# Kernel tuning notes

Hardware: AMD Instinct MI355X
Metric: run time of the kernel (lower is better)

Reference implementation:

```python
import jax, jax.numpy as jnp
import numpy as np

S, U, K, N_NEG, Z_DIM, C_DIM, LENGTH = 8, 8, 6, 17, 64, 256, 512
T = LENGTH + K


def setup_inputs() -> dict:
    key = jax.random.key(0)
    k1, k2, k3, k4, k5, k6 = jax.random.split(key, 6)
    z = jax.random.normal(k1, (S * U, T, Z_DIM), dtype=jnp.float32)
    c = jax.random.normal(k2, (S * U, T, C_DIM), dtype=jnp.float32)
    W = jax.random.normal(k3, (K, Z_DIM, C_DIM), dtype=jnp.float32) * 0.02
    b = jax.random.normal(k4, (K, Z_DIM), dtype=jnp.float32) * 0.02
    # torch: randint(0, U) per step
    batch_index = jax.random.randint(k5, (K, U, N_NEG), 0, U, dtype=jnp.int32)
    # torch: randint(1, length) + arange(length), mod length  (negative != positive at same pos)
    base = jax.random.randint(k6, (K, S, U, N_NEG, LENGTH), 1, LENGTH, dtype=jnp.int32)
    seq_index = (base + jnp.arange(LENGTH, dtype=jnp.int32)) % LENGTH
    return {"z": z, "c": c, "W": W, "b": b,
            "batch_index": batch_index, "seq_index": seq_index}


def reference(z, c, W, b, batch_index, seq_index):
    K_, zdim, _ = W.shape
    U_, n_neg = batch_index.shape[1], batch_index.shape[2]
    S_ = seq_index.shape[1]
    length = z.shape[1] - K_
    scale = 1.0 / float(np.sqrt(zdim))

    z_r = z.reshape(S_, U_, -1, zdim)              # [S,U,T,Z]
    c_s = c[:, :-K_, :].reshape(S_, U_, length, -1)  # [S,U,L,C]
    sp = jnp.arange(S_)[:, None, None, None]        # speaker index broadcast

    losses, accs = [], []
    for k in range(K_):  # fixed small number of prediction steps
        zs = z_r[:, :, k + 1:length + k + 1, :]                     # [S,U,L,Z]
        Wc = jnp.einsum('sulc,zc->sulz', c_s, W[k]) + b[k]          # predictor k
        f_pos = jnp.einsum('sulz,sulz->sul', zs, Wc) * scale        # [S,U,L]
        bi = batch_index[k][None, :, :, None]                       # [1,U,N,1]
        si = seq_index[k]                                           # [S,U,N,L]
        z_neg = zs[sp, bi, si, :]                                   # [S,U,N,L,Z]
        f_neg = jnp.einsum('sunlz,sulz->sunl', z_neg, Wc) * scale   # [S,U,N,L]
        f = jnp.concatenate([f_pos[:, :, None, :], f_neg], axis=2)  # [S,U,N+1,L]
        # cross entropy with label 0 along class axis
        losses.append(jnp.mean(jax.nn.logsumexpp(f, axis=2) if False else jax.nn.logsumexp(f, axis=2) - f_pos))
        accs.append(jnp.mean((jnp.argmax(f, axis=2) == 0).astype(jnp.float32)))

    loss = jnp.stack(losses).mean()
    return loss, jnp.stack(accs)
```

## Files before the change

### kernel.cpp

```cpp
#include <hip/hip_runtime.h>
#include <math.h>

#define S_N 8
#define U_N 8
#define K_N 6
#define NNEG 17
#define ZDIM 64
#define CDIM 256
#define LEN 512
#define TDIM (LEN + K_N)

typedef __attribute__((ext_vector_type(8))) short short8;
typedef __attribute__((ext_vector_type(4))) short short4v;
typedef __attribute__((ext_vector_type(4))) float f32x4;

__device__ __forceinline__ short f2bf(float x) {
    unsigned u = __builtin_bit_cast(unsigned, x);
    return (short)((u + 0x7fffu + ((u >> 16) & 1u)) >> 16);
}
__device__ __forceinline__ float bf2f(short h) {
    unsigned u = ((unsigned)(unsigned short)h) << 16;
    return __builtin_bit_cast(float, u);
}
__device__ __forceinline__ short8 cvt8(f32x4 a, f32x4 b) {
    short8 r;
    r[0] = f2bf(a[0]); r[1] = f2bf(a[1]); r[2] = f2bf(a[2]); r[3] = f2bf(a[3]);
    r[4] = f2bf(b[0]); r[5] = f2bf(b[1]); r[6] = f2bf(b[2]); r[7] = f2bf(b[3]);
    return r;
}


__global__ __launch_bounds__(256, 3) void cpc_gemm(
    const float* __restrict__ cg_, const float* __restrict__ Wg,
    const float* __restrict__ bg, short* __restrict__ Wcg)
{
    __shared__ __align__(16) short wlds[ZDIM * CDIM];
    __shared__ float wc[64][68];

    const int tid = threadIdx.x;
    const int bid = blockIdx.x;
    const int su  = bid >> 3;
    const int lt8 = bid & 7;
    const int l0  = lt8 * 64;

    const int wave   = tid >> 6;
    const int lane   = tid & 63;
    const int lane15 = lane & 15;
    const int lgrp   = lane >> 4;

    short8 af0, af1, af2, af3, af4, af5, af6, af7;
    {
        const int lrow = l0 + wave * 16 + lane15;
        const float* arow = cg_ + ((size_t)(su * TDIM + lrow)) * CDIM;
#define LDA(KC, AF) { \
        f32x4 a0_ = __builtin_nontemporal_load((const f32x4*)(arow + (KC) * 32 + lgrp * 8)); \
        f32x4 a1_ = __builtin_nontemporal_load((const f32x4*)(arow + (KC) * 32 + lgrp * 8 + 4)); \
        AF = cvt8(a0_, a1_); }
        LDA(0, af0) LDA(1, af1) LDA(2, af2) LDA(3, af3)
        LDA(4, af4) LDA(5, af5) LDA(6, af6) LDA(7, af7)
#undef LDA
    }

    for (int k = 0; k < K_N; ++k) {
        {
            const float* wbase = Wg + (size_t)k * ZDIM * CDIM;
            #pragma unroll
            for (int it = 0; it < 16; ++it) {
                int off = it * 1024 + tid * 4;
                int r = off >> 8;
                int c = off & 255;
                f32x4 v = *(const f32x4*)(wbase + off);
                short4v h;
                h.x = f2bf(v[0]); h.y = f2bf(v[1]); h.z = f2bf(v[2]); h.w = f2bf(v[3]);
                int chb = c >> 3;
                int hh  = (c >> 2) & 1;
                *(short4v*)&wlds[r * 256 + ((chb ^ (r & 7)) << 3) + hh * 4] = h;
            }
        }
        __syncthreads();

        {
            f32x4 acc0 = {0.f,0.f,0.f,0.f}, acc1 = {0.f,0.f,0.f,0.f};
            f32x4 acc2 = {0.f,0.f,0.f,0.f}, acc3 = {0.f,0.f,0.f,0.f};
            const int swb = lane15 & 7;
            const short* wl = &wlds[lane15 * 256];
#define DOKC(KC, AF) { \
            const int so = ((((KC) * 4 + lgrp) ^ swb) << 3); \
            acc0 = __builtin_amdgcn_mfma_f32_16x16x32_bf16(AF, *(const short8*)(wl + so),          acc0, 0, 0, 0); \
            acc1 = __builtin_amdgcn_mfma_f32_16x16x32_bf16(AF, *(const short8*)(wl + 16*256 + so), acc1, 0, 0, 0); \
            acc2 = __builtin_amdgcn_mfma_f32_16x16x32_bf16(AF, *(const short8*)(wl + 32*256 + so), acc2, 0, 0, 0); \
            acc3 = __builtin_amdgcn_mfma_f32_16x16x32_bf16(AF, *(const short8*)(wl + 48*256 + so), acc3, 0, 0, 0); }
            DOKC(0, af0) DOKC(1, af1) DOKC(2, af2) DOKC(3, af3)
            DOKC(4, af4) DOKC(5, af5) DOKC(6, af6) DOKC(7, af7)
#undef DOKC
            const int wrow = wave * 16 + lgrp * 4;
#define WCW(N, ACC) { \
            float bias_ = bg[k * ZDIM + (N) * 16 + lane15]; \
            wc[wrow + 0][(N) * 16 + lane15] = ACC[0] + bias_; \
            wc[wrow + 1][(N) * 16 + lane15] = ACC[1] + bias_; \
            wc[wrow + 2][(N) * 16 + lane15] = ACC[2] + bias_; \
            wc[wrow + 3][(N) * 16 + lane15] = ACC[3] + bias_; }
            WCW(0, acc0) WCW(1, acc1) WCW(2, acc2) WCW(3, acc3)
#undef WCW
        }
        __syncthreads();

        {
            const int row = tid >> 2;
            const int q   = tid & 3;
            f32x4 v0 = *(const f32x4*)&wc[row][q * 16];
            f32x4 v1 = *(const f32x4*)&wc[row][q * 16 + 4];
            f32x4 v2 = *(const f32x4*)&wc[row][q * 16 + 8];
            f32x4 v3 = *(const f32x4*)&wc[row][q * 16 + 12];
            short8 s0 = cvt8(v0, v1);
            short8 s1 = cvt8(v2, v3);
            short* dst = Wcg + (((size_t)(k * 64 + su) * LEN) + (l0 + row)) * ZDIM + q * 16;
            *(short8*)dst = s0;
            *(short8*)(dst + 8) = s1;
        }
    }
}


__global__ __launch_bounds__(256) void cpc_loss(
    const float* __restrict__ zg, const short* __restrict__ Wcg,
    const int* __restrict__ bidx, const int* __restrict__ sidx,
    float* __restrict__ bins)
{
    __shared__ int bi_sh[NNEG];
    __shared__ int si_sh[16 * NNEG];
    __shared__ float red[8];

    const int tid = threadIdx.x;
    const int bid = blockIdx.x;
    const int s   = bid & 7;
    const int b2  = bid >> 3;
    const int lt  = b2 & 31;
    const int u   = (b2 >> 5) & 7;
    const int k   = b2 >> 8;
    const int l0  = lt * 16;
    const int su  = s * 8 + u;

    if (tid < NNEG) bi_sh[tid] = bidx[(k * U_N + u) * NNEG + tid];
    for (int i = tid; i < 16 * NNEG; i += 256) {
        int lr = i / NNEG;
        int n  = i - lr * NNEG;
        si_sh[i] = sidx[((((size_t)k * S_N + s) * U_N + u) * NNEG + n) * LEN + (l0 + lr)];
    }
    __syncthreads();

    const int lrow = tid >> 4;
    const int c4   = tid & 15;
    const int l    = l0 + lrow;

    f32x4 wcv;
    {
        const short* wrow = Wcg + (((size_t)(k * 64 + su) * LEN) + l) * ZDIM + c4 * 4;
        short4v wb = __builtin_nontemporal_load((const short4v*)wrow);
        wcv[0] = bf2f(wb.x); wcv[1] = bf2f(wb.y); wcv[2] = bf2f(wb.z); wcv[3] = bf2f(wb.w);
    }

    float f0 = 0.f, mneg = -1e30f, se = 0.f;
    #pragma unroll 6
    for (int j = 0; j < 18; ++j) {
        size_t zrow;
        if (j == 0) {
            zrow = (size_t)su * TDIM + (k + 1 + l);
        } else {
            int n  = j - 1;
            int bi = bi_sh[n];
            int si = si_sh[lrow * NNEG + n];
            zrow = (size_t)(s * 8 + bi) * TDIM + (k + 1 + si);
        }
        f32x4 zv = *(const f32x4*)(zg + zrow * ZDIM + c4 * 4);
        float p = zv[0] * wcv[0];
        p = fmaf(zv[1], wcv[1], p);
        p = fmaf(zv[2], wcv[2], p);
        p = fmaf(zv[3], wcv[3], p);
        p += __shfl_xor(p, 1);
        p += __shfl_xor(p, 2);
        p += __shfl_xor(p, 4);
        p += __shfl_xor(p, 8);
        float f = p * 0.125f;
        if (j == 0) f0 = f; else mneg = fmaxf(mneg, f);
        se += __expf(f - 4.0f);
    }

    float lossv = (4.0f + __logf(se)) - f0;
    float accv  = (f0 >= mneg) ? 1.f : 0.f;
    if (c4 != 0) { lossv = 0.f; accv = 0.f; }
    lossv += __shfl_xor(lossv, 16); lossv += __shfl_xor(lossv, 32);
    accv  += __shfl_xor(accv, 16);  accv  += __shfl_xor(accv, 32);

    const int wave = tid >> 6;
    const int lane = tid & 63;
    if (lane == 0) { red[wave * 2] = lossv; red[wave * 2 + 1] = accv; }
    __syncthreads();
    if (tid == 0) atomicAdd(&bins[bid & 127], red[0] + red[2] + red[4] + red[6]);
    if (tid == 1) atomicAdd(&bins[128 + k * 128 + (bid & 127)],
                            red[1] + red[3] + red[5] + red[7]);
}

__global__ void cpc_final(const float* __restrict__ bins, float* __restrict__ out)
{
    const int lane = threadIdx.x;
    float v = bins[lane] + bins[lane + 64];
    #pragma unroll
    for (int off = 1; off < 64; off <<= 1) v += __shfl_xor(v, off);
    if (lane == 0) out[0] = v * (1.0f / 196608.0f);
    #pragma unroll
    for (int k = 0; k < K_N; ++k) {
        const float* bk = bins + 128 + k * 128;
        float a = bk[lane] + bk[lane + 64];
        #pragma unroll
        for (int off = 1; off < 64; off <<= 1) a += __shfl_xor(a, off);
        if (lane == 0) out[1 + k] = a * (1.0f / 32768.0f);
    }
}

__global__ __launch_bounds__(256, 3) void cpc_fused(
    const float* __restrict__ zg, const float* __restrict__ cg_,
    const float* __restrict__ Wg, const float* __restrict__ bg,
    const int* __restrict__ bidx, const int* __restrict__ sidx,
    float* __restrict__ out)
{
    __shared__ __align__(16) short wlds[ZDIM * CDIM];
    __shared__ float wc[64][68];
    __shared__ float lds_red[8];

    const int tid = threadIdx.x;
    const int bid = blockIdx.x;
    const int lb  = (bid & 7) * 64 + (bid >> 3);
    const int su  = lb >> 3;
    const int lt8 = lb & 7;
    const int s   = su >> 3;
    const int u   = su & 7;
    const int l0  = lt8 * 64;

    const int wave   = tid >> 6;
    const int lane   = tid & 63;
    const int lane15 = lane & 15;
    const int lgrp   = lane >> 4;

    if (tid < 8) lds_red[tid] = 0.f;

    short8 af0, af1, af2, af3, af4, af5, af6, af7;
    {
        const int lrow = l0 + wave * 16 + lane15;
        const float* arow = cg_ + ((size_t)(su * TDIM + lrow)) * CDIM;
#define LDA(KC, AF) { \
        f32x4 a0_ = *(const f32x4*)(arow + (KC) * 32 + lgrp * 8); \
        f32x4 a1_ = *(const f32x4*)(arow + (KC) * 32 + lgrp * 8 + 4); \
        AF = cvt8(a0_, a1_); }
        LDA(0, af0) LDA(1, af1) LDA(2, af2) LDA(3, af3)
        LDA(4, af4) LDA(5, af5) LDA(6, af6) LDA(7, af7)
#undef LDA
    }

    float loss_acc = 0.f;
    for (int k = 0; k < K_N; ++k) {
        {
            const float* wbase = Wg + (size_t)k * ZDIM * CDIM;
            #pragma unroll
            for (int it = 0; it < 16; ++it) {
                int off = it * 1024 + tid * 4;
                int r = off >> 8;
                int c = off & 255;
                f32x4 v = *(const f32x4*)(wbase + off);
                short4v h;
                h.x = f2bf(v[0]); h.y = f2bf(v[1]); h.z = f2bf(v[2]); h.w = f2bf(v[3]);
                *(short4v*)&wlds[r * 256 + (((c >> 3) ^ (r & 7)) << 3) + ((c >> 2) & 1) * 4] = h;
            }
        }
        __syncthreads();
        {
            f32x4 acc0 = {0.f,0.f,0.f,0.f}, acc1 = {0.f,0.f,0.f,0.f};
            f32x4 acc2 = {0.f,0.f,0.f,0.f}, acc3 = {0.f,0.f,0.f,0.f};
            const int swb = lane15 & 7;
            const short* wl = &wlds[lane15 * 256];
#define DOKC(KC, AF) { \
            const int so = ((((KC) * 4 + lgrp) ^ swb) << 3); \
            acc0 = __builtin_amdgcn_mfma_f32_16x16x32_bf16(AF, *(const short8*)(wl + so),          acc0, 0, 0, 0); \
            acc1 = __builtin_amdgcn_mfma_f32_16x16x32_bf16(AF, *(const short8*)(wl + 16*256 + so), acc1, 0, 0, 0); \
            acc2 = __builtin_amdgcn_mfma_f32_16x16x32_bf16(AF, *(const short8*)(wl + 32*256 + so), acc2, 0, 0, 0); \
            acc3 = __builtin_amdgcn_mfma_f32_16x16x32_bf16(AF, *(const short8*)(wl + 48*256 + so), acc3, 0, 0, 0); }
            DOKC(0, af0) DOKC(1, af1) DOKC(2, af2) DOKC(3, af3)
            DOKC(4, af4) DOKC(5, af5) DOKC(6, af6) DOKC(7, af7)
#undef DOKC
            const int wrow = wave * 16 + lgrp * 4;
#define WCW(N, ACC) { \
            float bias_ = bg[k * ZDIM + (N) * 16 + lane15]; \
            wc[wrow + 0][(N) * 16 + lane15] = ACC[0] + bias_; \
            wc[wrow + 1][(N) * 16 + lane15] = ACC[1] + bias_; \
            wc[wrow + 2][(N) * 16 + lane15] = ACC[2] + bias_; \
            wc[wrow + 3][(N) * 16 + lane15] = ACC[3] + bias_; }
            WCW(0, acc0) WCW(1, acc1) WCW(2, acc2) WCW(3, acc3)
#undef WCW
        }
        __syncthreads();

        const int lt = tid >> 2;
        const int jq = tid & 3;
        const int l  = l0 + lt;
        float fv[5];
        #pragma unroll
        for (int t = 0; t < 5; ++t) {
            int j = jq + 4 * t;
            if (j >= 18) { fv[t] = -1e30f; continue; }
            const float* zp;
            if (j == 0) {
                zp = zg + ((size_t)(su * TDIM + (k + 1 + l))) * ZDIM;
            } else {
                int n  = j - 1;
                int bi = bidx[(k * U_N + u) * NNEG + n];
                int si = sidx[(size_t)((((k * S_N + s) * U_N + u) * NNEG + n)) * LEN + l];
                zp = zg + ((size_t)((s * U_N + bi) * TDIM + (k + 1 + si))) * ZDIM;
            }
            float f = 0.f;
            const float* wr = &wc[lt][0];
            #pragma unroll
            for (int c4i = 0; c4i < 16; ++c4i) {
                f32x4 zv = *(const f32x4*)(zp + c4i * 4);
                f32x4 wv = *(const f32x4*)(wr + c4i * 4);
                f = fmaf(zv[0], wv[0], f); f = fmaf(zv[1], wv[1], f);
                f = fmaf(zv[2], wv[2], f); f = fmaf(zv[3], wv[3], f);
            }
            fv[t] = f * 0.125f;
        }
        float mall = -1e30f, mneg = -1e30f;
        #pragma unroll
        for (int t = 0; t < 5; ++t) {
            mall = fmaxf(mall, fv[t]);
            bool skip = (jq == 0 && t == 0) || (jq + 4 * t >= 18);
            if (!skip) mneg = fmaxf(mneg, fv[t]);
        }
        mall = fmaxf(mall, __shfl_xor(mall, 1));
        mall = fmaxf(mall, __shfl_xor(mall, 2));
        mneg = fmaxf(mneg, __shfl_xor(mneg, 1));
        mneg = fmaxf(mneg, __shfl_xor(mneg, 2));
        float se = 0.f;
        #pragma unroll
        for (int t = 0; t < 5; ++t)
            if (jq + 4 * t < 18) se += __expf(fv[t] - mall);
        se += __shfl_xor(se, 1);
        se += __shfl_xor(se, 2);
        float lossv = 0.f, accv = 0.f;
        if (jq == 0) {
            lossv = (mall + __logf(se)) - fv[0];
            accv  = (fv[0] >= mneg) ? 1.f : 0.f;
        }
        loss_acc += lossv;
        #pragma unroll
        for (int off = 1; off < 64; off <<= 1) accv += __shfl_xor(accv, off);
        if (lane == 0) atomicAdd(&lds_red[1 + k], accv);
    }
    #pragma unroll
    for (int off = 1; off < 64; off <<= 1) loss_acc += __shfl_xor(loss_acc, off);
    if (lane == 0) atomicAdd(&lds_red[0], loss_acc);
    __syncthreads();
    if (tid == 0) atomicAdd(out, lds_red[0] * (1.0f / 196608.0f));
    if (tid >= 8 && tid < 8 + K_N)
        atomicAdd(out + 1 + (tid - 8), lds_red[1 + (tid - 8)] * (1.0f / 32768.0f));
}

extern "C" void kernel_launch(void* const* d_in, const int* in_sizes, int n_in,
                              void* d_out, int out_size, void* d_ws, size_t ws_size,
                              hipStream_t stream) {
    const float* z = (const float*)d_in[0];
    const float* c = (const float*)d_in[1];
    const float* W = (const float*)d_in[2];
    const float* b = (const float*)d_in[3];
    const int* batch_index = (const int*)d_in[4];
    const int* seq_index   = (const int*)d_in[5];
    float* out = (float*)d_out;

    const size_t WCG_BYTES  = (size_t)K_N * 64 * LEN * ZDIM * sizeof(short);
    const size_t BINS_FLOATS = 7 * 128;

    if (ws_size >= WCG_BYTES + BINS_FLOATS * sizeof(float)) {
        short* Wcg  = (short*)d_ws;
        float* bins = (float*)((char*)d_ws + WCG_BYTES);
        hipMemsetAsync(bins, 0, BINS_FLOATS * sizeof(float), stream);
        cpc_gemm<<<dim3(512), dim3(256), 0, stream>>>(c, W, b, Wcg);
        cpc_loss<<<dim3(12288), dim3(256), 0, stream>>>(z, Wcg, batch_index, seq_index, bins);
        cpc_final<<<dim3(1), dim3(64), 0, stream>>>(bins, out);
    } else {
        hipMemsetAsync(out, 0, 7 * sizeof(float), stream);
        cpc_fused<<<dim3(512), dim3(256), 0, stream>>>(z, c, W, b, batch_index, seq_index, out);
    }
}
```

Before: 173.6 us.

## Restructure loss gather per quad with DPP reduce and pre-convert W to bf16

W is converted to bf16 once by a new small kernel, and the GEMM reads B fragments directly from global instead of staging into LDS. The GEMM now uses smaller 128-thread blocks and folds the 1/sqrt(z) scale into Wc. The loss kernel precomputes gather byte offsets in LDS and assigns 4-lane quads to distinct negatives with 16 elements per lane. It reduces with DPP instead of 4 shuffles per candidate. This adds a kernel launch and padded wasted iterations.

```diff
diff --git a/kernel.cpp b/kernel.cpp
--- a/kernel.cpp
+++ b/kernel.cpp
@@ -28,20 +28,34 @@
     r[4] = f2bf(b[0]); r[5] = f2bf(b[1]); r[6] = f2bf(b[2]); r[7] = f2bf(b[3]);
     return r;
 }
-
-
-__global__ __launch_bounds__(256, 3) void cpc_gemm(
-    const float* __restrict__ cg_, const float* __restrict__ Wg,
+__device__ __forceinline__ float qsum(float x) {
+    int i = __builtin_bit_cast(int, x);
+    float y = x + __builtin_bit_cast(float, __builtin_amdgcn_mov_dpp(i, 0xB1, 0xF, 0xF, true));
+    int i2 = __builtin_bit_cast(int, y);
+    return y + __builtin_bit_cast(float, __builtin_amdgcn_mov_dpp(i2, 0x4E, 0xF, 0xF, true));
+}
+
+__global__ __launch_bounds__(256) void cpc_wcvt(const float* __restrict__ Wg,
+                                                short* __restrict__ wbf)
+{
+    int i4 = (blockIdx.x * 256 + threadIdx.x) * 4;
+    f32x4 v = *(const f32x4*)(Wg + i4);
+    short4v h;
+    h.x = f2bf(v[0]); h.y = f2bf(v[1]); h.z = f2bf(v[2]); h.w = f2bf(v[3]);
+    *(short4v*)(wbf + i4) = h;
+}
+
+__global__ __launch_bounds__(128) void cpc_gemm(
+    const float* __restrict__ cg_, const short* __restrict__ wbf,
     const float* __restrict__ bg, short* __restrict__ Wcg)
 {
-    __shared__ __align__(16) short wlds[ZDIM * CDIM];
-    __shared__ float wc[64][68];
+    __shared__ float wc[32][68];
 
     const int tid = threadIdx.x;
     const int bid = blockIdx.x;
-    const int su  = bid >> 3;
-    const int lt8 = bid & 7;
-    const int l0  = lt8 * 64;
+    const int su  = bid >> 4;
+    const int lt16 = bid & 15;
+    const int l0  = lt16 * 32;
 
     const int wave   = tid >> 6;
     const int lane   = tid & 63;
@@ -62,49 +76,31 @@
     }
 
     for (int k = 0; k < K_N; ++k) {
-        {
-            const float* wbase = Wg + (size_t)k * ZDIM * CDIM;
-            #pragma unroll
-            for (int it = 0; it < 16; ++it) {
-                int off = it * 1024 + tid * 4;
-                int r = off >> 8;
-                int c = off & 255;
-                f32x4 v = *(const f32x4*)(wbase + off);
-                short4v h;
-                h.x = f2bf(v[0]); h.y = f2bf(v[1]); h.z = f2bf(v[2]); h.w = f2bf(v[3]);
-                int chb = c >> 3;
-                int hh  = (c >> 2) & 1;
-                *(short4v*)&wlds[r * 256 + ((chb ^ (r & 7)) << 3) + hh * 4] = h;
-            }
-        }
+        f32x4 acc0 = {0.f,0.f,0.f,0.f}, acc1 = {0.f,0.f,0.f,0.f};
+        f32x4 acc2 = {0.f,0.f,0.f,0.f}, acc3 = {0.f,0.f,0.f,0.f};
+        const short* wp0 = wbf + ((k * 64 + lane15) << 8) + lgrp * 8;
+#define DOKC(KC, AF) { \
+        short8 b0 = *(const short8*)(wp0 + (KC) * 32); \
+        short8 b1 = *(const short8*)(wp0 + (KC) * 32 + (16 << 8)); \
+        short8 b2 = *(const short8*)(wp0 + (KC) * 32 + (32 << 8)); \
+        short8 b3 = *(const short8*)(wp0 + (KC) * 32 + (48 << 8)); \
+        acc0 = __builtin_amdgcn_mfma_f32_16x16x32_bf16(AF, b0, acc0, 0, 0, 0); \
+        acc1 = __builtin_amdgcn_mfma_f32_16x16x32_bf16(AF, b1, acc1, 0, 0, 0); \
+        acc2 = __builtin_amdgcn_mfma_f32_16x16x32_bf16(AF, b2, acc2, 0, 0, 0); \
+        acc3 = __builtin_amdgcn_mfma_f32_16x16x32_bf16(AF, b3, acc3, 0, 0, 0); }
+        DOKC(0, af0) DOKC(1, af1) DOKC(2, af2) DOKC(3, af3)
+        DOKC(4, af4) DOKC(5, af5) DOKC(6, af6) DOKC(7, af7)
+#undef DOKC
+        const int wrow = wave * 16 + lgrp * 4;
+#define WCW(N, ACC) { \
+        float b025 = bg[k * ZDIM + (N) * 16 + lane15] * 0.125f; \
+        wc[wrow + 0][(N) * 16 + lane15] = fmaf(ACC[0], 0.125f, b025); \
+        wc[wrow + 1][(N) * 16 + lane15] = fmaf(ACC[1], 0.125f, b025); \
+        wc[wrow + 2][(N) * 16 + lane15] = fmaf(ACC[2], 0.125f, b025); \
+        wc[wrow + 3][(N) * 16 + lane15] = fmaf(ACC[3], 0.125f, b025); }
+        WCW(0, acc0) WCW(1, acc1) WCW(2, acc2) WCW(3, acc3)
+#undef WCW
         __syncthreads();
-
-        {
-            f32x4 acc0 = {0.f,0.f,0.f,0.f}, acc1 = {0.f,0.f,0.f,0.f};
-            f32x4 acc2 = {0.f,0.f,0.f,0.f}, acc3 = {0.f,0.f,0.f,0.f};
-            const int swb = lane15 & 7;
-            const short* wl = &wlds[lane15 * 256];
-#define DOKC(KC, AF) { \
-            const int so = ((((KC) * 4 + lgrp) ^ swb) << 3); \
-            acc0 = __builtin_amdgcn_mfma_f32_16x16x32_bf16(AF, *(const short8*)(wl + so),          acc0, 0, 0, 0); \
-            acc1 = __builtin_amdgcn_mfma_f32_16x16x32_bf16(AF, *(const short8*)(wl + 16*256 + so), acc1, 0, 0, 0); \
-            acc2 = __builtin_amdgcn_mfma_f32_16x16x32_bf16(AF, *(const short8*)(wl + 32*256 + so), acc2, 0, 0, 0); \
-            acc3 = __builtin_amdgcn_mfma_f32_16x16x32_bf16(AF, *(const short8*)(wl + 48*256 + so), acc3, 0, 0, 0); }
-            DOKC(0, af0) DOKC(1, af1) DOKC(2, af2) DOKC(3, af3)
-            DOKC(4, af4) DOKC(5, af5) DOKC(6, af6) DOKC(7, af7)
-#undef DOKC
-            const int wrow = wave * 16 + lgrp * 4;
-#define WCW(N, ACC) { \
-            float bias_ = bg[k * ZDIM + (N) * 16 + lane15]; \
-            wc[wrow + 0][(N) * 16 + lane15] = ACC[0] + bias_; \
-            wc[wrow + 1][(N) * 16 + lane15] = ACC[1] + bias_; \
-            wc[wrow + 2][(N) * 16 + lane15] = ACC[2] + bias_; \
-            wc[wrow + 3][(N) * 16 + lane15] = ACC[3] + bias_; }
-            WCW(0, acc0) WCW(1, acc1) WCW(2, acc2) WCW(3, acc3)
-#undef WCW
-        }
-        __syncthreads();
-
         {
             const int row = tid >> 2;
             const int q   = tid & 3;
@@ -118,17 +114,16 @@
             *(short8*)dst = s0;
             *(short8*)(dst + 8) = s1;
         }
-    }
-}
-
+        __syncthreads();
+    }
+}
 
 __global__ __launch_bounds__(256) void cpc_loss(
     const float* __restrict__ zg, const short* __restrict__ Wcg,
     const int* __restrict__ bidx, const int* __restrict__ sidx,
     float* __restrict__ bins)
 {
-    __shared__ int bi_sh[NNEG];
-    __shared__ int si_sh[16 * NNEG];
+    __shared__ unsigned offs[16 * 18];
     __shared__ float red[8];
 
     const int tid = threadIdx.x;
@@ -141,54 +136,75 @@
     const int l0  = lt * 16;
     const int su  = s * 8 + u;
 
-    if (tid < NNEG) bi_sh[tid] = bidx[(k * U_N + u) * NNEG + tid];
-    for (int i = tid; i < 16 * NNEG; i += 256) {
-        int lr = i / NNEG;
-        int n  = i - lr * NNEG;
-        si_sh[i] = sidx[((((size_t)k * S_N + s) * U_N + u) * NNEG + n) * LEN + (l0 + lr)];
-    }
-    __syncthreads();
-
-    const int lrow = tid >> 4;
-    const int c4   = tid & 15;
-    const int l    = l0 + lrow;
-
-    f32x4 wcv;
-    {
-        const short* wrow = Wcg + (((size_t)(k * 64 + su) * LEN) + l) * ZDIM + c4 * 4;
-        short4v wb = __builtin_nontemporal_load((const short4v*)wrow);
-        wcv[0] = bf2f(wb.x); wcv[1] = bf2f(wb.y); wcv[2] = bf2f(wb.z); wcv[3] = bf2f(wb.w);
-    }
-
-    float f0 = 0.f, mneg = -1e30f, se = 0.f;
-    #pragma unroll 6
-    for (int j = 0; j < 18; ++j) {
-        size_t zrow;
+    for (int i = tid; i < 288; i += 256) {
+        int lr = i & 15;
+        int j  = i >> 4;
+        int l  = l0 + lr;
+        unsigned row;
         if (j == 0) {
-            zrow = (size_t)su * TDIM + (k + 1 + l);
+            row = (unsigned)(su * TDIM + (k + 1 + l));
         } else {
             int n  = j - 1;
-            int bi = bi_sh[n];
-            int si = si_sh[lrow * NNEG + n];
-            zrow = (size_t)(s * 8 + bi) * TDIM + (k + 1 + si);
-        }
-        f32x4 zv = *(const f32x4*)(zg + zrow * ZDIM + c4 * 4);
-        float p = zv[0] * wcv[0];
-        p = fmaf(zv[1], wcv[1], p);
-        p = fmaf(zv[2], wcv[2], p);
-        p = fmaf(zv[3], wcv[3], p);
-        p += __shfl_xor(p, 1);
-        p += __shfl_xor(p, 2);
-        p += __shfl_xor(p, 4);
-        p += __shfl_xor(p, 8);
-        float f = p * 0.125f;
-        if (j == 0) f0 = f; else mneg = fmaxf(mneg, f);
+            int bi = bidx[(k * U_N + u) * NNEG + n];
+            int si = sidx[((((size_t)k * S_N + s) * U_N + u) * NNEG + n) * LEN + l];
+            row = (unsigned)((s * 8 + bi) * TDIM + (k + 1 + si));
+        }
+        offs[lr * 18 + j] = row * (ZDIM * 4);
+    }
+    __syncthreads();
+
+    const int lrow  = tid >> 4;
+    const int c4    = tid & 15;
+    const int quad  = c4 >> 2;
+    const int qlane = c4 & 3;
+    const int l     = l0 + lrow;
+
+    f32x4 w0, w1, w2, w3;
+    {
+        const short* wr = Wcg + (((size_t)(k * 64 + su) * LEN) + l) * ZDIM + qlane * 16;
+        short8 h0 = *(const short8*)wr;
+        short8 h1 = *(const short8*)(wr + 8);
+        w0[0]=bf2f(h0[0]); w0[1]=bf2f(h0[1]); w0[2]=bf2f(h0[2]); w0[3]=bf2f(h0[3]);
+        w1[0]=bf2f(h0[4]); w1[1]=bf2f(h0[5]); w1[2]=bf2f(h0[6]); w1[3]=bf2f(h0[7]);
+        w2[0]=bf2f(h1[0]); w2[1]=bf2f(h1[1]); w2[2]=bf2f(h1[2]); w2[3]=bf2f(h1[3]);
+        w3[0]=bf2f(h1[4]); w3[1]=bf2f(h1[5]); w3[2]=bf2f(h1[6]); w3[3]=bf2f(h1[7]);
+    }
+
+    const char* zb = (const char*)zg;
+    float f0 = 0.f, mneg = -1e30f, se = 0.f;
+    #pragma unroll
+    for (int jr = 0; jr < 5; ++jr) {
+        int j  = jr * 4 + quad;
+        int jc = (j < 18) ? j : 17;
+        unsigned off = offs[lrow * 18 + jc];
+        const float* zp = (const float*)(zb + off) + qlane * 16;
+        f32x4 z0 = *(const f32x4*)(zp);
+        f32x4 z1 = *(const f32x4*)(zp + 4);
+        f32x4 z2 = *(const f32x4*)(zp + 8);
+        f32x4 z3 = *(const f32x4*)(zp + 12);
+        float p = z0[0] * w0[0];
+        p = fmaf(z0[1], w0[1], p); p = fmaf(z0[2], w0[2], p); p = fmaf(z0[3], w0[3], p);
+        p = fmaf(z1[0], w1[0], p); p = fmaf(z1[1], w1[1], p);
+        p = fmaf(z1[2], w1[2], p); p = fmaf(z1[3], w1[3], p);
+        p = fmaf(z2[0], w2[0], p); p = fmaf(z2[1], w2[1], p);
+        p = fmaf(z2[2], w2[2], p); p = fmaf(z2[3], w2[3], p);
+        p = fmaf(z3[0], w3[0], p); p = fmaf(z3[1], w3[1], p);
+        p = fmaf(z3[2], w3[2], p); p = fmaf(z3[3], w3[3], p);
+        float f = qsum(p);
+        if (j >= 18) f = -1e30f;
+        if (j == 0) f0 = f;
+        else        mneg = fmaxf(mneg, f);
         se += __expf(f - 4.0f);
     }
-
-    float lossv = (4.0f + __logf(se)) - f0;
-    float accv  = (f0 >= mneg) ? 1.f : 0.f;
-    if (c4 != 0) { lossv = 0.f; accv = 0.f; }
+    se += __shfl_xor(se, 4);  se += __shfl_xor(se, 8);
+    mneg = fmaxf(mneg, __shfl_xor(mneg, 4));
+    mneg = fmaxf(mneg, __shfl_xor(mneg, 8));
+
+    float lossv = 0.f, accv = 0.f;
+    if (c4 == 0) {
+        lossv = (4.0f + __logf(se)) - f0;
+        accv  = (f0 >= mneg) ? 1.f : 0.f;
+    }
     lossv += __shfl_xor(lossv, 16); lossv += __shfl_xor(lossv, 32);
     accv  += __shfl_xor(accv, 16);  accv  += __shfl_xor(accv, 32);
 
@@ -374,14 +390,17 @@
     const int* seq_index   = (const int*)d_in[5];
     float* out = (float*)d_out;
 
+    const size_t WBF_BYTES  = (size_t)K_N * ZDIM * CDIM * sizeof(short);
     const size_t WCG_BYTES  = (size_t)K_N * 64 * LEN * ZDIM * sizeof(short);
     const size_t BINS_FLOATS = 7 * 128;
 
-    if (ws_size >= WCG_BYTES + BINS_FLOATS * sizeof(float)) {
-        short* Wcg  = (short*)d_ws;
-        float* bins = (float*)((char*)d_ws + WCG_BYTES);
+    if (ws_size >= WBF_BYTES + WCG_BYTES + BINS_FLOATS * sizeof(float)) {
+        short* wbf  = (short*)d_ws;
+        short* Wcg  = (short*)((char*)d_ws + WBF_BYTES);
+        float* bins = (float*)((char*)d_ws + WBF_BYTES + WCG_BYTES);
         hipMemsetAsync(bins, 0, BINS_FLOATS * sizeof(float), stream);
-        cpc_gemm<<<dim3(512), dim3(256), 0, stream>>>(c, W, b, Wcg);
+        cpc_wcvt<<<dim3(96), dim3(256), 0, stream>>>(W, wbf);
+        cpc_gemm<<<dim3(1024), dim3(128), 0, stream>>>(c, wbf, b, Wcg);
         cpc_loss<<<dim3(12288), dim3(256), 0, stream>>>(z, Wcg, batch_index, seq_index, bins);
         cpc_final<<<dim3(1), dim3(64), 0, stream>>>(bins, out);
     } else {
```

Result: slower. 226.1 us (+30.3%).

## Pre-convert W to bf16, fold scale into Wc, use DPP row reduction

Applied to the files above, without the earlier changes.

A new small kernel converts W to bf16 once, so each of the 512 GEMM blocks loads half the bytes and skips per-block conversion when filling LDS. The 1/sqrt(Z) scale is folded into the Wc epilogue. The loss kernel's 16-lane shuffle reduction is replaced with DPP moves. A missing end-of-iteration barrier in the GEMM's k loop is added, which fixes a possible LDS race on the wc tile but adds a sync per step. The cost is one extra kernel launch and a small workspace buffer.

```diff
diff --git a/kernel.cpp b/kernel.cpp
--- a/kernel.cpp
+++ b/kernel.cpp
@@ -28,10 +28,30 @@
     r[4] = f2bf(b[0]); r[5] = f2bf(b[1]); r[6] = f2bf(b[2]); r[7] = f2bf(b[3]);
     return r;
 }
-
+__device__ __forceinline__ float sum16(float x) {
+    int a = __builtin_bit_cast(int, x);
+    float y = x + __builtin_bit_cast(float, __builtin_amdgcn_mov_dpp(a, 0xB1, 0xF, 0xF, true));
+    a = __builtin_bit_cast(int, y);
+    y = y + __builtin_bit_cast(float, __builtin_amdgcn_mov_dpp(a, 0x4E, 0xF, 0xF, true));
+    a = __builtin_bit_cast(int, y);
+    y = y + __builtin_bit_cast(float, __builtin_amdgcn_mov_dpp(a, 0x141, 0xF, 0xF, true));
+    a = __builtin_bit_cast(int, y);
+    y = y + __builtin_bit_cast(float, __builtin_amdgcn_mov_dpp(a, 0x140, 0xF, 0xF, true));
+    return y;
+}
+
+__global__ __launch_bounds__(256) void cpc_wcvt(const float* __restrict__ Wg,
+                                                short* __restrict__ wbf)
+{
+    int i4 = (blockIdx.x * 256 + threadIdx.x) * 4;
+    f32x4 v = *(const f32x4*)(Wg + i4);
+    short4v h;
+    h.x = f2bf(v[0]); h.y = f2bf(v[1]); h.z = f2bf(v[2]); h.w = f2bf(v[3]);
+    *(short4v*)(wbf + i4) = h;
+}
 
 __global__ __launch_bounds__(256, 3) void cpc_gemm(
-    const float* __restrict__ cg_, const float* __restrict__ Wg,
+    const float* __restrict__ cg_, const short* __restrict__ wbf,
     const float* __restrict__ bg, short* __restrict__ Wcg)
 {
     __shared__ __align__(16) short wlds[ZDIM * CDIM];
@@ -63,18 +83,14 @@
 
     for (int k = 0; k < K_N; ++k) {
         {
-            const float* wbase = Wg + (size_t)k * ZDIM * CDIM;
+            const short* wkb = wbf + k * (ZDIM * CDIM);
             #pragma unroll
-            for (int it = 0; it < 16; ++it) {
-                int off = it * 1024 + tid * 4;
-                int r = off >> 8;
-                int c = off & 255;
-                f32x4 v = *(const f32x4*)(wbase + off);
-                short4v h;
-                h.x = f2bf(v[0]); h.y = f2bf(v[1]); h.z = f2bf(v[2]); h.w = f2bf(v[3]);
-                int chb = c >> 3;
-                int hh  = (c >> 2) & 1;
-                *(short4v*)&wlds[r * 256 + ((chb ^ (r & 7)) << 3) + hh * 4] = h;
+            for (int it = 0; it < 8; ++it) {
+                int ch = it * 256 + tid;
+                int r  = ch >> 5;
+                int cc = ch & 31;
+                short8 h = *(const short8*)(wkb + r * 256 + cc * 8);
+                *(short8*)&wlds[r * 256 + ((cc ^ (r & 7)) << 3)] = h;
             }
         }
         __syncthreads();
@@ -95,11 +111,11 @@
 #undef DOKC
             const int wrow = wave * 16 + lgrp * 4;
 #define WCW(N, ACC) { \
-            float bias_ = bg[k * ZDIM + (N) * 16 + lane15]; \
-            wc[wrow + 0][(N) * 16 + lane15] = ACC[0] + bias_; \
-            wc[wrow + 1][(N) * 16 + lane15] = ACC[1] + bias_; \
-            wc[wrow + 2][(N) * 16 + lane15] = ACC[2] + bias_; \
-            wc[wrow + 3][(N) * 16 + lane15] = ACC[3] + bias_; }
+            float b025 = bg[k * ZDIM + (N) * 16 + lane15] * 0.125f; \
+            wc[wrow + 0][(N) * 16 + lane15] = fmaf(ACC[0], 0.125f, b025); \
+            wc[wrow + 1][(N) * 16 + lane15] = fmaf(ACC[1], 0.125f, b025); \
+            wc[wrow + 2][(N) * 16 + lane15] = fmaf(ACC[2], 0.125f, b025); \
+            wc[wrow + 3][(N) * 16 + lane15] = fmaf(ACC[3], 0.125f, b025); }
             WCW(0, acc0) WCW(1, acc1) WCW(2, acc2) WCW(3, acc3)
 #undef WCW
         }
@@ -118,9 +134,9 @@
             *(short8*)dst = s0;
             *(short8*)(dst + 8) = s1;
         }
-    }
-}
-
+        __syncthreads();
+    }
+}
 
 __global__ __launch_bounds__(256) void cpc_loss(
     const float* __restrict__ zg, const short* __restrict__ Wcg,
@@ -177,11 +193,7 @@
         p = fmaf(zv[1], wcv[1], p);
         p = fmaf(zv[2], wcv[2], p);
         p = fmaf(zv[3], wcv[3], p);
-        p += __shfl_xor(p, 1);
-        p += __shfl_xor(p, 2);
-        p += __shfl_xor(p, 4);
-        p += __shfl_xor(p, 8);
-        float f = p * 0.125f;
+        float f = sum16(p);
         if (j == 0) f0 = f; else mneg = fmaxf(mneg, f);
         se += __expf(f - 4.0f);
     }
@@ -374,14 +386,17 @@
     const int* seq_index   = (const int*)d_in[5];
     float* out = (float*)d_out;
 
+    const size_t WBF_BYTES  = (size_t)K_N * ZDIM * CDIM * sizeof(short);
     const size_t WCG_BYTES  = (size_t)K_N * 64 * LEN * ZDIM * sizeof(short);
     const size_t BINS_FLOATS = 7 * 128;
 
-    if (ws_size >= WCG_BYTES + BINS_FLOATS * sizeof(float)) {
-        short* Wcg  = (short*)d_ws;
-        float* bins = (float*)((char*)d_ws + WCG_BYTES);
+    if (ws_size >= WBF_BYTES + WCG_BYTES + BINS_FLOATS * sizeof(float)) {
+        short* wbf  = (short*)d_ws;
+        short* Wcg  = (short*)((char*)d_ws + WBF_BYTES);
+        float* bins = (float*)((char*)d_ws + WBF_BYTES + WCG_BYTES);
         hipMemsetAsync(bins, 0, BINS_FLOATS * sizeof(float), stream);
-        cpc_gemm<<<dim3(512), dim3(256), 0, stream>>>(c, W, b, Wcg);
+        cpc_wcvt<<<dim3(96), dim3(256), 0, stream>>>(W, wbf);
+        cpc_gemm<<<dim3(512), dim3(256), 0, stream>>>(c, wbf, b, Wcg);
         cpc_loss<<<dim3(12288), dim3(256), 0, stream>>>(z, Wcg, batch_index, seq_index, bins);
         cpc_final<<<dim3(1), dim3(64), 0, stream>>>(bins, out);
     } else {
```

Result: faster. 164.9 us (-5.0%).
